# Optimization experiments

Hardware: AMD Instinct MI355X
Metric: run time of the kernel (lower is better)

Reference implementation:

```python
import jax, jax.numpy as jnp
import numpy as np

def setup_inputs() -> dict:
    key = jax.random.key(0)
    k1, k2 = jax.random.split(key)
    pcs1 = jax.random.normal(k1, (8, 4096, 3), dtype=jnp.float32)
    pcs2 = jax.random.normal(k2, (8, 4096, 3), dtype=jnp.float32)
    return {"pcs1": pcs1, "pcs2": pcs2}

def reference(pcs1, pcs2):
    # Pairwise squared L2 distances: [B, N, M]
    # ||a-b||^2 = ||a||^2 + ||b||^2 - 2 a.b
    sq1 = jnp.sum(pcs1 * pcs1, axis=-1)                # [B, N]
    sq2 = jnp.sum(pcs2 * pcs2, axis=-1)                # [B, M]
    inner = jnp.einsum('bnd,bmd->bnm', pcs1, pcs2)     # [B, N, M]
    d = sq1[:, :, None] + sq2[:, None, :] - 2.0 * inner
    d = jnp.maximum(d, 0.0)  # guard tiny negatives from cancellation
    dist1 = jnp.min(d, axis=2)   # [B, N] nearest in pcs2 for each point of pcs1
    dist2 = jnp.min(d, axis=1)   # [B, M] nearest in pcs1 for each point of pcs2
    loss1 = jnp.mean(jnp.sqrt(dist1))
    loss2 = jnp.mean(jnp.sqrt(dist2))
    return (loss1 + loss2) * 0.5
```

## Files before the change

### kernel.cpp

```cpp
#include <hip/hip_runtime.h>
#include <math.h>


typedef __attribute__((ext_vector_type(8)))  short bf16x8;
typedef __attribute__((ext_vector_type(16))) float f32x16;
typedef float f32x2 __attribute__((ext_vector_type(2)));

#define NPTS 4096
#define BATCH 8
#define FRAG_PER_B 8192u

union FragCast { uint4 u; bf16x8 v; };

__device__ __forceinline__ unsigned short f2bf(float f) {
    unsigned u = __float_as_uint(f);
    return (unsigned short)((u + 0x7FFFu + ((u >> 16) & 1u)) >> 16);
}
__device__ __forceinline__ float bf2f(unsigned short h) {
    return __uint_as_float(((unsigned)h) << 16);
}
__device__ __forceinline__ unsigned pk(unsigned short a, unsigned short b) {
    return (unsigned)a | ((unsigned)b << 16);
}

__global__ __launch_bounds__(256) void chamfer_prep(
    const float* __restrict__ pcs1, const float* __restrict__ pcs2,
    uint4* __restrict__ fa1, uint4* __restrict__ fa2,
    uint4* __restrict__ fb1, uint4* __restrict__ fb2,
    unsigned* __restrict__ dist)
{
    const int gid   = blockIdx.x * 256 + threadIdx.x;
    const int cloud = gid >> 15;
    const int idx   = gid & 32767;
    const int b     = idx >> 12;
    const int pt    = idx & 4095;

    dist[gid] = 0x7F800000u;

    const float* src = (cloud ? pcs2 : pcs1) + ((size_t)b * NPTS + pt) * 3;
    float x = src[0], y = src[1], z = src[2];
    float sq = fmaf(x, x, fmaf(y, y, z * z));

    float m2x = -2.0f * x, m2y = -2.0f * y, m2z = -2.0f * z;
    unsigned short hx = f2bf(m2x), hy = f2bf(m2y), hz = f2bf(m2z);
    unsigned short lx = f2bf(m2x - bf2f(hx));
    unsigned short ly = f2bf(m2y - bf2f(hy));
    unsigned short lz = f2bf(m2z - bf2f(hz));
    unsigned short sh = f2bf(sq);
    unsigned short sl = f2bf(sq - bf2f(sh));

    unsigned short px = f2bf(x), py = f2bf(y), pz = f2bf(z);
    unsigned short qx = f2bf(x - bf2f(px));
    unsigned short qy = f2bf(y - bf2f(py));
    unsigned short qz = f2bf(z - bf2f(pz));
    const unsigned short ONE = 0x3F80;

    uint4 a0 = make_uint4(pk(hx, hy), pk(hz, hx), pk(hy, hz), pk(lx, ly));
    uint4 a1 = make_uint4(pk(lz, lx), pk(ly, lz), pk(sh, sl), pk(ONE, ONE));
    uint4 b0 = make_uint4(pk(px, py), pk(pz, qx), pk(qy, qz), pk(px, py));
    uint4 b1 = make_uint4(pk(pz, qx), pk(qy, qz), pk(ONE, ONE), pk(sh, sl));

    const int tile = pt >> 5, row = pt & 31;
    const size_t i0 = (size_t)b * FRAG_PER_B + ((size_t)tile * 2 + 0) * 32 + row;
    const size_t i1 = (size_t)b * FRAG_PER_B + ((size_t)tile * 2 + 1) * 32 + row;
    uint4* fa = cloud ? fa2 : fa1;
    uint4* fb = cloud ? fb2 : fb1;
    fa[i0] = a0; fa[i1] = a1;
    fb[i0] = b0; fb[i1] = b1;
}

__global__ __launch_bounds__(256, 4) void chamfer_mfma(
    const uint4* __restrict__ fa1, const uint4* __restrict__ fa2,
    const uint4* __restrict__ fb1, const uint4* __restrict__ fb2,
    unsigned* __restrict__ dist)
{
    __shared__ uint4 stage[2048];

    const int bid  = blockIdx.x;
    const int dir  = bid >> 9;
    const int b    = (bid >> 6) & 7;
    const int mch  = (bid >> 1) & 31;
    const int half = bid & 1;

    const uint4* fA = (dir ? fa1 : fa2) + (size_t)b * FRAG_PER_B
                      + (size_t)half * 4096;
    const uint4* fB = (dir ? fb2 : fb1) + (size_t)b * FRAG_PER_B;

    const int tid = threadIdx.x;
    const int w   = tid >> 6;
    const int l   = tid & 63;
    const int hf  = l >> 5;
    const int ln  = l & 31;
    const int mtile = mch * 4 + w;

    FragCast bq;
    bq.u = fB[((size_t)mtile * 2 + hf) * 32 + ln];

    const f32x16 cz = {0.f,0.f,0.f,0.f,0.f,0.f,0.f,0.f,
                       0.f,0.f,0.f,0.f,0.f,0.f,0.f,0.f};
    float acc0 = 3.4e38f, acc1 = 3.4e38f;

    for (int phase = 0; phase < 2; ++phase) {
        __syncthreads();
#pragma unroll
        for (int i = 0; i < 8; ++i)
            stage[i * 256 + tid] = fA[(size_t)phase * 2048 + i * 256 + tid];
        __syncthreads();

#pragma unroll 2
        for (int j2 = 0; j2 < 16; ++j2) {
            FragCast aq0, aq1;
            aq0.u = stage[(j2 * 4 + 0 + hf) * 32 + ln];
            aq1.u = stage[(j2 * 4 + 2 + hf) * 32 + ln];
            f32x16 D0 = __builtin_amdgcn_mfma_f32_32x32x16_bf16(
                aq0.v, bq.v, cz, 0, 0, 0);
            f32x16 D1 = __builtin_amdgcn_mfma_f32_32x32x16_bf16(
                aq1.v, bq.v, cz, 0, 0, 0);
#pragma unroll
            for (int i = 0; i < 8; ++i)
                acc0 = fminf(fminf(acc0, D0[2 * i]), D0[2 * i + 1]);
#pragma unroll
            for (int i = 0; i < 8; ++i)
                acc1 = fminf(fminf(acc1, D1[2 * i]), D1[2 * i + 1]);
        }
    }

    float accmin = fminf(acc0, acc1);
    accmin = fminf(accmin, __shfl_xor(accmin, 32, 64));

    if (l < 32) {
        const int col = mtile * 32 + ln;
        float d = fmaxf(accmin, 0.0f);
        atomicMin(&dist[(((unsigned)dir * 8 + b) << 12) + col],
                  __float_as_uint(d));
    }
}

__global__ __launch_bounds__(256) void chamfer_red1(
    const unsigned* __restrict__ dist, float* __restrict__ bpart)
{
    __shared__ float ws[4];
    const int t = threadIdx.x;
    const uint4* d4 = (const uint4*)dist;
    uint4 v = d4[blockIdx.x * 256 + t];
    float s = sqrtf(__uint_as_float(v.x)) + sqrtf(__uint_as_float(v.y))
            + sqrtf(__uint_as_float(v.z)) + sqrtf(__uint_as_float(v.w));
#pragma unroll
    for (int off = 1; off < 64; off <<= 1) s += __shfl_xor(s, off, 64);
    if ((t & 63) == 0) ws[t >> 6] = s;
    __syncthreads();
    if (t == 0)
        bpart[blockIdx.x] = ws[0] + ws[1] + ws[2] + ws[3];
}

__global__ __launch_bounds__(64) void chamfer_red2(
    const float* __restrict__ bpart, float* __restrict__ out)
{
    float v = bpart[threadIdx.x];
#pragma unroll
    for (int off = 1; off < 64; off <<= 1) v += __shfl_xor(v, off, 64);
    if (threadIdx.x == 0) out[0] = v * (1.0f / 65536.0f);
}

#define CPAIRS 1024
#define PA 16
#define RSTRIDE 68

__device__ __forceinline__ f32x2 pk_fma_lo(f32x2 c, f32x2 q, f32x2 acc) {
    f32x2 d;
    asm("v_pk_fma_f32 %0, %1, %2, %3 op_sel:[0,0,0] op_sel_hi:[0,1,1]"
        : "=v"(d) : "v"(c), "v"(q), "v"(acc));
    return d;
}
__device__ __forceinline__ f32x2 pk_fma_hi(f32x2 c, f32x2 q, f32x2 acc) {
    f32x2 d;
    asm("v_pk_fma_f32 %0, %1, %2, %3 op_sel:[1,0,0] op_sel_hi:[1,1,1]"
        : "=v"(d) : "v"(c), "v"(q), "v"(acc));
    return d;
}
__device__ __forceinline__ void vmin3(float& acc, float a, float b) {
    asm("v_min3_f32 %0, %1, %2, %3" : "=v"(acc) : "v"(acc), "v"(a), "v"(b));
}

__global__ __launch_bounds__(256, 4) void chamfer_vec(
    const float* __restrict__ pcs1, const float* __restrict__ pcs2,
    float* __restrict__ partials)
{
    __shared__ float4 lds[2 * CPAIRS];
    float4* bx = lds;
    float4* bz = lds + CPAIRS;

    const int bid = blockIdx.x;
    const int dir = bid >> 9;
    const int b   = (bid >> 6) & 7;
    const int ach = bid & 63;

    const float* A  = dir ? pcs2 : pcs1;
    const float* Bp = dir ? pcs1 : pcs2;
    const float* abase = A  + (size_t)b * NPTS * 3;
    const float* bbase = Bp + (size_t)b * NPTS * 3;

    const int tid = threadIdx.x;
    const int w   = tid >> 6;
    const int l   = tid & 63;

    const int apt = ach * 64 + w * PA;
    f32x2 cx[PA / 2], cy[PA / 2], cz2[PA / 2];
    float tmin[PA];
#pragma unroll
    for (int p2 = 0; p2 < PA / 2; ++p2) {
        const float* s = abase + (size_t)(apt + 2 * p2) * 3;
        cx[p2]  = (f32x2){-2.0f * s[0], -2.0f * s[3]};
        cy[p2]  = (f32x2){-2.0f * s[1], -2.0f * s[4]};
        cz2[p2] = (f32x2){-2.0f * s[2], -2.0f * s[5]};
        tmin[2 * p2] = 3.4e38f; tmin[2 * p2 + 1] = 3.4e38f;
    }

    for (int c = 0; c < 2; ++c) {
        if (c) __syncthreads();
#pragma unroll
        for (int i = 0; i < CPAIRS / 256; ++i) {
            int j  = i * 256 + tid;
            const float* s = bbase + (size_t)(c * CPAIRS + j) * 6;
            float x0 = s[0], y0 = s[1], z0 = s[2];
            float x1 = s[3], y1 = s[4], z1 = s[5];
            bx[j] = make_float4(x0, x1, y0, y1);
            bz[j] = make_float4(z0, z1,
                                fmaf(x0, x0, fmaf(y0, y0, z0 * z0)),
                                fmaf(x1, x1, fmaf(y1, y1, z1 * z1)));
        }
        __syncthreads();
#pragma unroll 4
        for (int t = 0; t < CPAIRS / 64; ++t) {
            float4 X = bx[t * 64 + l];
            float4 Z = bz[t * 64 + l];
            f32x2 qx = (f32x2){X.x, X.y};
            f32x2 qy = (f32x2){X.z, X.w};
            f32x2 qz = (f32x2){Z.x, Z.y};
            f32x2 qw = (f32x2){Z.z, Z.w};
#pragma unroll
            for (int p2 = 0; p2 < PA / 2; ++p2) {
                f32x2 d0 = pk_fma_lo(cz2[p2], qz, qw);
                d0 = pk_fma_lo(cy[p2], qy, d0);
                d0 = pk_fma_lo(cx[p2], qx, d0);
                vmin3(tmin[2 * p2], d0.x, d0.y);
                f32x2 d1 = pk_fma_hi(cz2[p2], qz, qw);
                d1 = pk_fma_hi(cy[p2], qy, d1);
                d1 = pk_fma_hi(cx[p2], qx, d1);
                vmin3(tmin[2 * p2 + 1], d1.x, d1.y);
            }
        }
    }

    __syncthreads();
    float* lds2 = (float*)lds;
#pragma unroll
    for (int p = 0; p < PA; ++p)
        lds2[(w * PA + p) * RSTRIDE + l] = tmin[p];
    __syncthreads();

    if (tid < 64) {
        const int g = tid;
        float m = 3.4e38f;
        const float4* row = (const float4*)&lds2[g * RSTRIDE];
#pragma unroll
        for (int i = 0; i < 16; ++i) {
            float4 v = row[i];
            m = fminf(fminf(m, fminf(v.x, v.y)), fminf(v.z, v.w));
        }
        const int ap = ach * 64 + g;
        float x = abase[ap * 3 + 0], y = abase[ap * 3 + 1], z = abase[ap * 3 + 2];
        float s = sqrtf(fmaxf(fmaf(x, x, fmaf(y, y, z * z)) + m, 0.0f));
#pragma unroll
        for (int off = 1; off < 64; off <<= 1) s += __shfl_xor(s, off, 64);
        if (g == 0) partials[bid] = s;
    }
}

__global__ __launch_bounds__(256) void chamfer_final(
    const float* __restrict__ partials, int n, float scale,
    float* __restrict__ out)
{
    __shared__ float ws[4];
    const int t = threadIdx.x;
    float v = 0.0f;
    for (int i = t; i < n; i += 256) v += partials[i];
#pragma unroll
    for (int off = 1; off < 64; off <<= 1) v += __shfl_xor(v, off, 64);
    if ((t & 63) == 0) ws[t >> 6] = v;
    __syncthreads();
    if (t == 0)
        out[0] = (ws[0] + ws[1] + ws[2] + ws[3]) * scale;
}

extern "C" void kernel_launch(void* const* d_in, const int* in_sizes, int n_in,
                              void* d_out, int out_size, void* d_ws, size_t ws_size,
                              hipStream_t stream) {
    const float* pcs1 = (const float*)d_in[0];
    const float* pcs2 = (const float*)d_in[1];
    float* out = (float*)d_out;

    const size_t MB = 1048576;
    const size_t need = 4 * MB + 256 * 1024 + 1024;

    if (ws_size >= need) {
        char* w = (char*)d_ws;
        uint4* fa1 = (uint4*)(w + 0 * MB);
        uint4* fa2 = (uint4*)(w + 1 * MB);
        uint4* fb1 = (uint4*)(w + 2 * MB);
        uint4* fb2 = (uint4*)(w + 3 * MB);
        unsigned* dist = (unsigned*)(w + 4 * MB);
        float* bpart   = (float*)(w + 4 * MB + 256 * 1024);

        chamfer_prep<<<dim3(256),  dim3(256), 0, stream>>>(
            pcs1, pcs2, fa1, fa2, fb1, fb2, dist);
        chamfer_mfma<<<dim3(1024), dim3(256), 0, stream>>>(
            fa1, fa2, fb1, fb2, dist);
        chamfer_red1<<<dim3(64),   dim3(256), 0, stream>>>(dist, bpart);
        chamfer_red2<<<dim3(1),    dim3(64),  0, stream>>>(bpart, out);
    } else {
        float* partials = (float*)d_ws;
        chamfer_vec  <<<dim3(1024), dim3(256), 0, stream>>>(pcs1, pcs2, partials);
        chamfer_final<<<dim3(1),    dim3(256), 0, stream>>>(
            partials, 1024, 1.0f / 65536.0f, out);
    }
}
```

Baseline: 23.02 us.

## Compute distance matrix once and reduce both row and column minima from it

Before, the MFMA distance tiles were computed twice, once per direction, and each pass kept only column minima. Now each block computes every tile once and extracts both minima from it. Row minima are kept in registers, reduced with shuffles and written out with global atomicMin. Column minima are combined with LDS atomics into per-block partials, which the reduction kernel then folds. This halves MFMA work and prep output, at the cost of per-tile LDS atomics, more registers, and an extra partial-min buffer to read in the reduction.

```diff
diff --git a/kernel.cpp b/kernel.cpp
--- a/kernel.cpp
+++ b/kernel.cpp
@@ -25,126 +25,148 @@
 
 __global__ __launch_bounds__(256) void chamfer_prep(
     const float* __restrict__ pcs1, const float* __restrict__ pcs2,
-    uint4* __restrict__ fa1, uint4* __restrict__ fa2,
-    uint4* __restrict__ fb1, uint4* __restrict__ fb2,
-    unsigned* __restrict__ dist)
-{
-    const int gid   = blockIdx.x * 256 + threadIdx.x;
-    const int cloud = gid >> 15;
-    const int idx   = gid & 32767;
-    const int b     = idx >> 12;
-    const int pt    = idx & 4095;
-
-    dist[gid] = 0x7F800000u;
-
-    const float* src = (cloud ? pcs2 : pcs1) + ((size_t)b * NPTS + pt) * 3;
-    float x = src[0], y = src[1], z = src[2];
-    float sq = fmaf(x, x, fmaf(y, y, z * z));
-
-    float m2x = -2.0f * x, m2y = -2.0f * y, m2z = -2.0f * z;
-    unsigned short hx = f2bf(m2x), hy = f2bf(m2y), hz = f2bf(m2z);
-    unsigned short lx = f2bf(m2x - bf2f(hx));
-    unsigned short ly = f2bf(m2y - bf2f(hy));
-    unsigned short lz = f2bf(m2z - bf2f(hz));
-    unsigned short sh = f2bf(sq);
-    unsigned short sl = f2bf(sq - bf2f(sh));
-
-    unsigned short px = f2bf(x), py = f2bf(y), pz = f2bf(z);
-    unsigned short qx = f2bf(x - bf2f(px));
-    unsigned short qy = f2bf(y - bf2f(py));
-    unsigned short qz = f2bf(z - bf2f(pz));
-    const unsigned short ONE = 0x3F80;
-
-    uint4 a0 = make_uint4(pk(hx, hy), pk(hz, hx), pk(hy, hz), pk(lx, ly));
-    uint4 a1 = make_uint4(pk(lz, lx), pk(ly, lz), pk(sh, sl), pk(ONE, ONE));
-    uint4 b0 = make_uint4(pk(px, py), pk(pz, qx), pk(qy, qz), pk(px, py));
-    uint4 b1 = make_uint4(pk(pz, qx), pk(qy, qz), pk(ONE, ONE), pk(sh, sl));
+    uint4* __restrict__ fa1, uint4* __restrict__ fb2,
+    unsigned* __restrict__ dist1u)
+{
+    const int gid = blockIdx.x * 256 + threadIdx.x;
+    const int b   = gid >> 12;
+    const int pt  = gid & 4095;
+
+    dist1u[gid] = 0x7F800000u;
 
     const int tile = pt >> 5, row = pt & 31;
     const size_t i0 = (size_t)b * FRAG_PER_B + ((size_t)tile * 2 + 0) * 32 + row;
     const size_t i1 = (size_t)b * FRAG_PER_B + ((size_t)tile * 2 + 1) * 32 + row;
-    uint4* fa = cloud ? fa2 : fa1;
-    uint4* fb = cloud ? fb2 : fb1;
-    fa[i0] = a0; fa[i1] = a1;
-    fb[i0] = b0; fb[i1] = b1;
-}
-
-__global__ __launch_bounds__(256, 4) void chamfer_mfma(
-    const uint4* __restrict__ fa1, const uint4* __restrict__ fa2,
-    const uint4* __restrict__ fb1, const uint4* __restrict__ fb2,
-    unsigned* __restrict__ dist)
-{
-    __shared__ uint4 stage[2048];
-
-    const int bid  = blockIdx.x;
-    const int dir  = bid >> 9;
-    const int b    = (bid >> 6) & 7;
-    const int mch  = (bid >> 1) & 31;
-    const int half = bid & 1;
-
-    const uint4* fA = (dir ? fa1 : fa2) + (size_t)b * FRAG_PER_B
-                      + (size_t)half * 4096;
-    const uint4* fB = (dir ? fb2 : fb1) + (size_t)b * FRAG_PER_B;
+    const unsigned short ONE = 0x3F80;
+
+    {
+        const float* s = pcs1 + ((size_t)b * NPTS + pt) * 3;
+        float x = s[0], y = s[1], z = s[2];
+        float sq = fmaf(x, x, fmaf(y, y, z * z));
+        float m2x = -2.0f * x, m2y = -2.0f * y, m2z = -2.0f * z;
+        unsigned short hx = f2bf(m2x), hy = f2bf(m2y), hz = f2bf(m2z);
+        unsigned short lx = f2bf(m2x - bf2f(hx));
+        unsigned short ly = f2bf(m2y - bf2f(hy));
+        unsigned short lz = f2bf(m2z - bf2f(hz));
+        unsigned short sh = f2bf(sq);
+        unsigned short sl = f2bf(sq - bf2f(sh));
+        fa1[i0] = make_uint4(pk(hx, hy), pk(hz, hx), pk(hy, hz), pk(lx, ly));
+        fa1[i1] = make_uint4(pk(lz, lx), pk(ly, lz), pk(sh, sl), pk(ONE, ONE));
+    }
+    {
+        const float* s = pcs2 + ((size_t)b * NPTS + pt) * 3;
+        float x = s[0], y = s[1], z = s[2];
+        float sq = fmaf(x, x, fmaf(y, y, z * z));
+        unsigned short px = f2bf(x), py = f2bf(y), pz = f2bf(z);
+        unsigned short qx = f2bf(x - bf2f(px));
+        unsigned short qy = f2bf(y - bf2f(py));
+        unsigned short qz = f2bf(z - bf2f(pz));
+        unsigned short sh = f2bf(sq);
+        unsigned short sl = f2bf(sq - bf2f(sh));
+        fb2[i0] = make_uint4(pk(px, py), pk(pz, qx), pk(qy, qz), pk(px, py));
+        fb2[i1] = make_uint4(pk(pz, qx), pk(qy, qz), pk(ONE, ONE), pk(sh, sl));
+    }
+}
+
+__global__ __launch_bounds__(512, 2) void chamfer_mfma(
+    const uint4* __restrict__ fa1, const uint4* __restrict__ fb2,
+    unsigned* __restrict__ dist1u, unsigned* __restrict__ cpart)
+{
+    __shared__ unsigned ldscol[2048];
+
+    const int bid    = blockIdx.x;
+    const int b      = bid >> 5;
+    const int rgroup = (bid >> 1) & 15;
+    const int chalf  = bid & 1;
 
     const int tid = threadIdx.x;
     const int w   = tid >> 6;
     const int l   = tid & 63;
     const int hf  = l >> 5;
     const int ln  = l & 31;
-    const int mtile = mch * 4 + w;
-
-    FragCast bq;
-    bq.u = fB[((size_t)mtile * 2 + hf) * 32 + ln];
+    const int rt  = rgroup * 8 + w;
+
+    {
+        uint4* lc4 = (uint4*)ldscol;
+        lc4[tid] = make_uint4(0x7F800000u, 0x7F800000u, 0x7F800000u, 0x7F800000u);
+    }
+
+    FragCast aq;
+    aq.u = fa1[(size_t)b * FRAG_PER_B + ((size_t)rt * 2 + hf) * 32 + ln];
+
+    const uint4* bptr = fb2 + (size_t)b * FRAG_PER_B
+                        + (size_t)chalf * 64 * 64 + hf * 32 + ln;
 
     const f32x16 cz = {0.f,0.f,0.f,0.f,0.f,0.f,0.f,0.f,
                        0.f,0.f,0.f,0.f,0.f,0.f,0.f,0.f};
-    float acc0 = 3.4e38f, acc1 = 3.4e38f;
-
-    for (int phase = 0; phase < 2; ++phase) {
-        __syncthreads();
-#pragma unroll
-        for (int i = 0; i < 8; ++i)
-            stage[i * 256 + tid] = fA[(size_t)phase * 2048 + i * 256 + tid];
-        __syncthreads();
-
+    float rmin[16];
+#pragma unroll
+    for (int i = 0; i < 16; ++i) rmin[i] = 3.4e38f;
+
+    __syncthreads();
+
+    uint4 p0 = bptr[0];
+    uint4 p1 = bptr[64];
 #pragma unroll 2
-        for (int j2 = 0; j2 < 16; ++j2) {
-            FragCast aq0, aq1;
-            aq0.u = stage[(j2 * 4 + 0 + hf) * 32 + ln];
-            aq1.u = stage[(j2 * 4 + 2 + hf) * 32 + ln];
-            f32x16 D0 = __builtin_amdgcn_mfma_f32_32x32x16_bf16(
-                aq0.v, bq.v, cz, 0, 0, 0);
-            f32x16 D1 = __builtin_amdgcn_mfma_f32_32x32x16_bf16(
-                aq1.v, bq.v, cz, 0, 0, 0);
-#pragma unroll
-            for (int i = 0; i < 8; ++i)
-                acc0 = fminf(fminf(acc0, D0[2 * i]), D0[2 * i + 1]);
-#pragma unroll
-            for (int i = 0; i < 8; ++i)
-                acc1 = fminf(fminf(acc1, D1[2 * i]), D1[2 * i + 1]);
-        }
-    }
-
-    float accmin = fminf(acc0, acc1);
-    accmin = fminf(accmin, __shfl_xor(accmin, 32, 64));
-
-    if (l < 32) {
-        const int col = mtile * 32 + ln;
-        float d = fmaxf(accmin, 0.0f);
-        atomicMin(&dist[(((unsigned)dir * 8 + b) << 12) + col],
-                  __float_as_uint(d));
+    for (int ct = 0; ct < 64; ++ct) {
+        FragCast bq; bq.u = p0;
+        p0 = p1;
+        p1 = bptr[(size_t)(ct + 2) * 64];
+        f32x16 D = __builtin_amdgcn_mfma_f32_32x32x16_bf16(aq.v, bq.v, cz, 0, 0, 0);
+
+#pragma unroll
+        for (int i = 0; i < 16; ++i) rmin[i] = fminf(rmin[i], D[i]);
+
+        float cm = fminf(D[0], D[1]);
+#pragma unroll
+        for (int i = 1; i < 8; ++i)
+            cm = fminf(fminf(cm, D[2 * i]), D[2 * i + 1]);
+        cm = fmaxf(cm, 0.0f);
+        atomicMin(&ldscol[ct * 32 + ln], __float_as_uint(cm));
+    }
+
+#pragma unroll
+    for (int off = 1; off < 32; off <<= 1) {
+#pragma unroll
+        for (int i = 0; i < 16; ++i)
+            rmin[i] = fminf(rmin[i], __shfl_xor(rmin[i], off, 64));
+    }
+    float v = 3.4e38f;
+#pragma unroll
+    for (int reg = 0; reg < 16; ++reg)
+        if (ln == reg) v = rmin[reg];
+    if (ln < 16) {
+        const int row = (ln & 3) + 8 * (ln >> 2) + 4 * hf;
+        atomicMin(&dist1u[(size_t)b * NPTS + rt * 32 + row],
+                  __float_as_uint(fmaxf(v, 0.0f)));
+    }
+
+    __syncthreads();
+    {
+        const uint4* lc4 = (const uint4*)ldscol;
+        uint4* dst = (uint4*)&cpart[(((size_t)(b * 2 + chalf) * 16 + rgroup) * 2048)];
+        dst[tid] = lc4[tid];
     }
 }
 
 __global__ __launch_bounds__(256) void chamfer_red1(
-    const unsigned* __restrict__ dist, float* __restrict__ bpart)
+    const unsigned* __restrict__ dist1u, const unsigned* __restrict__ cpart,
+    float* __restrict__ bpart)
 {
     __shared__ float ws[4];
-    const int t = threadIdx.x;
-    const uint4* d4 = (const uint4*)dist;
-    uint4 v = d4[blockIdx.x * 256 + t];
-    float s = sqrtf(__uint_as_float(v.x)) + sqrtf(__uint_as_float(v.y))
-            + sqrtf(__uint_as_float(v.z)) + sqrtf(__uint_as_float(v.w));
+    const int t  = threadIdx.x;
+    const int tg = blockIdx.x * 256 + t;
+    const int b  = tg >> 12;
+    const int c  = tg & 4095;
+    const int chalf = c >> 11, cl = c & 2047;
+
+    unsigned m = 0xFFFFFFFFu;
+    const unsigned* base = &cpart[(size_t)(b * 2 + chalf) * 16 * 2048 + cl];
+#pragma unroll
+    for (int rg = 0; rg < 16; ++rg)
+        m = min(m, base[(size_t)rg * 2048]);
+
+    float s = sqrtf(__uint_as_float(m)) + sqrtf(__uint_as_float(dist1u[tg]));
 #pragma unroll
     for (int off = 1; off < 64; off <<= 1) s += __shfl_xor(s, off, 64);
     if ((t & 63) == 0) ws[t >> 6] = s;
@@ -156,7 +178,7 @@
 __global__ __launch_bounds__(64) void chamfer_red2(
     const float* __restrict__ bpart, float* __restrict__ out)
 {
-    float v = bpart[threadIdx.x];
+    float v = bpart[threadIdx.x] + bpart[threadIdx.x + 64];
 #pragma unroll
     for (int off = 1; off < 64; off <<= 1) v += __shfl_xor(v, off, 64);
     if (threadIdx.x == 0) out[0] = v * (1.0f / 65536.0f);
@@ -301,23 +323,22 @@
     float* out = (float*)d_out;
 
     const size_t MB = 1048576;
-    const size_t need = 4 * MB + 256 * 1024 + 1024;
+    const size_t need = 2 * MB + 128 * 1024 + 2 * MB + 4096;
 
     if (ws_size >= need) {
         char* w = (char*)d_ws;
-        uint4* fa1 = (uint4*)(w + 0 * MB);
-        uint4* fa2 = (uint4*)(w + 1 * MB);
-        uint4* fb1 = (uint4*)(w + 2 * MB);
-        uint4* fb2 = (uint4*)(w + 3 * MB);
-        unsigned* dist = (unsigned*)(w + 4 * MB);
-        float* bpart   = (float*)(w + 4 * MB + 256 * 1024);
-
-        chamfer_prep<<<dim3(256),  dim3(256), 0, stream>>>(
-            pcs1, pcs2, fa1, fa2, fb1, fb2, dist);
-        chamfer_mfma<<<dim3(1024), dim3(256), 0, stream>>>(
-            fa1, fa2, fb1, fb2, dist);
-        chamfer_red1<<<dim3(64),   dim3(256), 0, stream>>>(dist, bpart);
-        chamfer_red2<<<dim3(1),    dim3(64),  0, stream>>>(bpart, out);
+        uint4*    fa1    = (uint4*)(w);
+        uint4*    fb2    = (uint4*)(w + 1 * MB);
+        unsigned* dist1u = (unsigned*)(w + 2 * MB);
+        unsigned* cpart  = (unsigned*)(w + 2 * MB + 128 * 1024);
+        float*    bpart  = (float*)(w + 4 * MB + 128 * 1024);
+
+        chamfer_prep<<<dim3(128), dim3(256), 0, stream>>>(
+            pcs1, pcs2, fa1, fb2, dist1u);
+        chamfer_mfma<<<dim3(256), dim3(512), 0, stream>>>(
+            fa1, fb2, dist1u, cpart);
+        chamfer_red1<<<dim3(128), dim3(256), 0, stream>>>(dist1u, cpart, bpart);
+        chamfer_red2<<<dim3(1),   dim3(64),  0, stream>>>(bpart, out);
     } else {
         float* partials = (float*)d_ws;
         chamfer_vec  <<<dim3(1024), dim3(256), 0, stream>>>(pcs1, pcs2, partials);
```

Measured after the change: 28.05 us. +21.9%, slower.
